# Kernel optimization log

Measured on AMD Instinct MI355X. Metric: run time of the kernel, lower is better.

Reference implementation:

```python
import jax, jax.numpy as jnp
import numpy as np

B = 8          # number of subgraphs (seq_start_end rows)
N = 2048       # nodes per subgraph (equal-size segments)
D = 64         # h_dim
H = 4          # gat_heads
ALPHA = 0.2    # leaky relu slope


def setup_inputs() -> dict:
    key = jax.random.key(0)
    k1, k2, k3, k4, k5 = jax.random.split(key, 5)
    h_states = jax.random.normal(k1, (B * N, D), dtype=jnp.float32)
    # xavier-ish scales
    W_heads = jax.random.normal(k2, (H, D, D), dtype=jnp.float32) * (1.414 * np.sqrt(2.0 / (D + D)))
    a_heads = jax.random.normal(k3, (H, 2 * D), dtype=jnp.float32) * (1.414 * np.sqrt(2.0 / (2 * D + 1)))
    W_out = jax.random.normal(k4, (H * D, D), dtype=jnp.float32) * (1.414 * np.sqrt(2.0 / (H * D + D)))
    a_out = jax.random.normal(k5, (2 * D,), dtype=jnp.float32) * (1.414 * np.sqrt(2.0 / (2 * D + 1)))
    starts = jnp.arange(B, dtype=jnp.int32) * N
    seq_start_end = jnp.stack([starts, starts + N], axis=1)  # (B, 2)
    return {"h_states": h_states, "W_heads": W_heads, "a_heads": a_heads,
            "W_out": W_out, "a_out": a_out, "seq_start_end": seq_start_end}


def _gat_layer(x, W, a):
    """Dense GAT layer. Equivalent to the torch.cat O(N^2*2d) construction,
    rewritten as separate a1/a2 projections + broadcast add. Eval mode (no dropout)."""
    h = x @ W                      # (N, dout)
    d = W.shape[1]
    s1 = h @ a[:d]                 # (N,)  score contribution of source node i
    s2 = h @ a[d:]                 # (N,)  score contribution of target node j
    e = jax.nn.leaky_relu(s1[:, None] + s2[None, :], ALPHA)  # (N, N)
    attn = jax.nn.softmax(e, axis=1)
    return attn @ h                # (N, dout)


def reference(h_states, W_heads, a_heads, W_out, a_out, seq_start_end):
    # seq_start_end encodes B equal contiguous segments of length N -> reshape
    x = h_states.reshape(B, N, D)

    def per_graph(xg):  # xg: (N, D)
        # multi-head attention layers, concat=True -> elu on each head output
        hp = jax.vmap(lambda W, a: jax.nn.elu(_gat_layer(xg, W, a)))(W_heads, a_heads)  # (H, N, D)
        xc = jnp.transpose(hp, (1, 0, 2)).reshape(N, H * D)
        # output attention layer, concat=False (no elu inside), then elu + log_softmax outside
        out = jax.nn.elu(_gat_layer(xc, W_out, a_out))   # (N, D)
        return jax.nn.log_softmax(out, axis=1)

    return jax.vmap(per_graph)(x).reshape(B * N, D)
```

## Files before the change

kernel.cpp:

```cpp
#include <hip/hip_runtime.h>
#include <math.h>

#define NTOT 16384
#define NSEG 2048

#define OFF_HH   0ull
#define OFF_XC   4194304ull
#define OFF_S1H  8388608ull
#define OFF_S2H  8454144ull
#define OFF_S1O  8519680ull
#define OFF_S2O  8536064ull
#define OFF_SVAL 8552448ull
#define OFF_WN   8617984ull
#define OFF_SIDX 8683520ull
#define OFF_VAS  8749056ull
#define OFF_CSA  9277440ull
#define OFF_CSS  9281568ull
#define OFF_SCA  9285696ull
#define OFF_SCS  9351232ull
#define OFF_AS   9416768ull

__device__ inline unsigned long long pack_key(float v, int idx) {
    unsigned u = __float_as_uint(v);
    u = (u & 0x80000000u) ? ~u : (u | 0x80000000u);
    return ((unsigned long long)u << 32) | (unsigned)idx;
}
__device__ inline float unpack_key(unsigned long long k) {
    unsigned u = (unsigned)(k >> 32);
    u = (u & 0x80000000u) ? (u ^ 0x80000000u) : ~u;
    return __uint_as_float(u);
}
__device__ inline unsigned long long shfl_xor_u64(unsigned long long x, int mask) {
    unsigned lo = (unsigned)x, hi = (unsigned)(x >> 32);
    lo = (unsigned)__shfl_xor((int)lo, mask, 64);
    hi = (unsigned)__shfl_xor((int)hi, mask, 64);
    return ((unsigned long long)hi << 32) | lo;
}

__global__ __launch_bounds__(256) void gemm1_k(const float* __restrict__ X,
                                               const float* __restrict__ Wh,
                                               const float* __restrict__ aH,
                                               float* __restrict__ hh,
                                               float* __restrict__ s1h,
                                               float* __restrict__ s2h) {
    __shared__ float As[64][68];
    __shared__ float Bs[64][68];
    const int tid = threadIdx.x;
    const int bm = blockIdx.x, h = blockIdx.y;
    const int c0 = tid & 63, r0 = tid >> 6;
#pragma unroll
    for (int r = 0; r < 16; ++r) {
        int row = r0 + r * 4;
        As[c0][row] = X[(size_t)(bm * 64 + row) * 64 + c0];
        Bs[row][c0] = Wh[h * 4096 + row * 64 + c0];
    }
    __syncthreads();
    const int tx = tid & 15, ty = tid >> 4;
    const int m0 = ty * 4, n0 = tx * 4;
    float acc[4][4] = {};
#pragma unroll
    for (int kk = 0; kk < 64; ++kk) {
        float4 a = *(const float4*)&As[kk][m0];
        float4 b = *(const float4*)&Bs[kk][n0];
        acc[0][0] += a.x * b.x; acc[0][1] += a.x * b.y; acc[0][2] += a.x * b.z; acc[0][3] += a.x * b.w;
        acc[1][0] += a.y * b.x; acc[1][1] += a.y * b.y; acc[1][2] += a.y * b.z; acc[1][3] += a.y * b.w;
        acc[2][0] += a.z * b.x; acc[2][1] += a.z * b.y; acc[2][2] += a.z * b.z; acc[2][3] += a.z * b.w;
        acc[3][0] += a.w * b.x; acc[3][1] += a.w * b.y; acc[3][2] += a.w * b.z; acc[3][3] += a.w * b.w;
    }
    const int g = bm >> 5;
    const int nb = (bm * 64) & 2047;
#pragma unroll
    for (int i = 0; i < 4; ++i) {
        float4 v = make_float4(acc[i][0], acc[i][1], acc[i][2], acc[i][3]);
        *(float4*)&hh[(((size_t)h * 8 + g) * NSEG + nb + m0 + i) * 64 + n0] = v;
    }
#pragma unroll
    for (int i = 0; i < 4; ++i) {
        float p1 = 0.f, p2 = 0.f;
#pragma unroll
        for (int jj = 0; jj < 4; ++jj) {
            p1 += acc[i][jj] * aH[h * 128 + n0 + jj];
            p2 += acc[i][jj] * aH[h * 128 + 64 + n0 + jj];
        }
#pragma unroll
        for (int off = 8; off; off >>= 1) {
            p1 += __shfl_xor(p1, off, 16);
            p2 += __shfl_xor(p2, off, 16);
        }
        if (tx == 0) {
            s1h[h * NTOT + bm * 64 + m0 + i] = p1;
            s2h[h * NTOT + bm * 64 + m0 + i] = p2;
        }
    }
}

__global__ __launch_bounds__(256) void gemm2_k(const float* __restrict__ XC,
                                               const float* __restrict__ Wo,
                                               const float* __restrict__ aO,
                                               float* __restrict__ hc,
                                               float* __restrict__ s1o,
                                               float* __restrict__ s2o) {
    __shared__ float As[64][34];
    __shared__ float Bs[64][68];
    const int tid = threadIdx.x;
    const int bm = blockIdx.x;
    const int c0 = tid & 63, r0 = tid >> 6;
    const int tx = tid & 15, ty = tid >> 4;
    const int m0 = ty * 2, n0 = tx * 4;
    float acc[2][4] = {};
    for (int kt = 0; kt < 4; ++kt) {
#pragma unroll
        for (int r = 0; r < 8; ++r) {
            int row = r0 + r * 4;
            As[c0][row] = XC[(size_t)(bm * 32 + row) * 256 + kt * 64 + c0];
        }
#pragma unroll
        for (int r = 0; r < 16; ++r) {
            int row = r0 + r * 4;
            Bs[row][c0] = Wo[(kt * 64 + row) * 64 + c0];
        }
        __syncthreads();
#pragma unroll
        for (int kk = 0; kk < 64; ++kk) {
            float2 a = *(const float2*)&As[kk][m0];
            float4 b = *(const float4*)&Bs[kk][n0];
            acc[0][0] += a.x * b.x; acc[0][1] += a.x * b.y; acc[0][2] += a.x * b.z; acc[0][3] += a.x * b.w;
            acc[1][0] += a.y * b.x; acc[1][1] += a.y * b.y; acc[1][2] += a.y * b.z; acc[1][3] += a.y * b.w;
        }
        __syncthreads();
    }
#pragma unroll
    for (int i = 0; i < 2; ++i) {
        float4 v = make_float4(acc[i][0], acc[i][1], acc[i][2], acc[i][3]);
        *(float4*)&hc[(size_t)(bm * 32 + m0 + i) * 64 + n0] = v;
    }
#pragma unroll
    for (int i = 0; i < 2; ++i) {
        float p1 = 0.f, p2 = 0.f;
#pragma unroll
        for (int jj = 0; jj < 4; ++jj) {
            p1 += acc[i][jj] * aO[n0 + jj];
            p2 += acc[i][jj] * aO[64 + n0 + jj];
        }
#pragma unroll
        for (int off = 8; off; off >>= 1) {
            p1 += __shfl_xor(p1, off, 16);
            p2 += __shfl_xor(p2, off, 16);
        }
        if (tx == 0) {
            s1o[bm * 32 + m0 + i] = p1;
            s2o[bm * 32 + m0 + i] = p2;
        }
    }
}

__global__ __launch_bounds__(1024) void sort_k(const float* __restrict__ s2_all,
                                               int heads,
                                               float* __restrict__ g_sval,
                                               int* __restrict__ g_sidx,
                                               float* __restrict__ g_wN) {
    __shared__ unsigned long long sA[2][1024];
    __shared__ unsigned long long sB[2][1024];
    __shared__ float sM2;
    const int tid = threadIdx.x, t = blockIdx.x;
    const int g = t / heads, h = t % heads;
    const float* s2p = s2_all + (size_t)h * NTOT + (size_t)g * NSEG;

    unsigned long long a0 = pack_key(s2p[tid], tid);
    unsigned long long a1 = pack_key(s2p[tid + 1024], tid + 1024);
    int p = 0;
    for (int k = 2; k <= 2048; k <<= 1) {
        const bool up0 = (tid & k) == 0;
        const bool up1 = (((tid + 1024) & k) == 0);
        for (int j = k >> 1; j > 0; j >>= 1) {
            if (j >= 1024) {
                unsigned long long lo = a0 < a1 ? a0 : a1;
                unsigned long long hi = a0 < a1 ? a1 : a0;
                a0 = up0 ? lo : hi;
                a1 = up0 ? hi : lo;
            } else if (j >= 64) {
                sA[p][tid] = a0; sB[p][tid] = a1;
                __syncthreads();
                unsigned long long q0 = sA[p][tid ^ j], q1 = sB[p][tid ^ j];
                bool lower = (tid & j) == 0;
                a0 = ((a0 < q0) == (lower == up0)) ? a0 : q0;
                a1 = ((a1 < q1) == (lower == up1)) ? a1 : q1;
                p ^= 1;
            } else {
                unsigned long long q0 = shfl_xor_u64(a0, j);
                unsigned long long q1 = shfl_xor_u64(a1, j);
                bool lower = (tid & j) == 0;
                a0 = ((a0 < q0) == (lower == up0)) ? a0 : q0;
                a1 = ((a1 < q1) == (lower == up1)) ? a1 : q1;
            }
        }
    }
    float v0 = unpack_key(a0), v1 = unpack_key(a1);
    if (tid == 1023) sM2 = v1;
    __syncthreads();
    const float M2 = sM2;
    int i0 = (int)(unsigned)(a0 & 0xffffffffu);
    int i1 = (int)(unsigned)(a1 & 0xffffffffu);
    float w0 = __expf(0.2f * (v0 - M2));
    float w1 = __expf(0.2f * (v1 - M2));
    size_t o = (size_t)t * NSEG;
    g_sval[o + tid] = v0; g_sval[o + tid + 1024] = v1;
    g_sidx[o + tid] = i0; g_sidx[o + tid + 1024] = i1;
    g_wN[o + tid] = w0;   g_wN[o + tid + 1024] = w1;
}

__global__ __launch_bounds__(256) void tabw_k(const float* __restrict__ V,
                                              int heads, int ntask,
                                              const int* __restrict__ g_sidx,
                                              const float* __restrict__ g_wN,
                                              float* __restrict__ AS,
                                              float* __restrict__ SCA, float* __restrict__ SCS,
                                              float* __restrict__ TAS,
                                              float* __restrict__ TSA, float* __restrict__ TSS) {
    const int L = blockIdx.x + (int)(gridDim.x * blockIdx.y);
    const int xcd = L & 7, slot = L >> 3;
    const int tpx = ntask >> 3;
    const int t = xcd * tpx + (slot >> 5);
    const int u = slot & 31;
    const int wv = threadIdx.x >> 6, lane = threadIdx.x & 63;
    const int c = u * 4 + wv, base = c * 16;
    const int g = t / heads, h = t % heads;
    const int seg = h * (ntask / heads) + g;
    const float* Vp = V + (size_t)seg * NSEG * 64;
    const int* sidx = g_sidx + (size_t)t * NSEG + base;
    const float* wnp = g_wN + (size_t)t * NSEG + base;
    float wn[16], vv[16];
#pragma unroll
    for (int j = 0; j < 16; ++j) wn[j] = wnp[j];
#pragma unroll
    for (int j = 0; j < 16; ++j) vv[j] = Vp[(size_t)sidx[j] * 64 + lane];
    float* ASp = AS + (size_t)t * NSEG * 128;
    float accA = 0.f, scaA = 0.f;
#pragma unroll
    for (int j = 0; j < 16; ++j) {
        size_t pos = base + j;
        ASp[pos * 128 + lane] = accA;
        if (lane == 0) SCA[(size_t)t * NSEG + pos] = scaA;
        accA += wn[j] * vv[j]; scaA += wn[j];
    }
    TAS[((size_t)t * 128 + c) * 128 + lane] = accA;
    if (lane == 0) TSA[t * 128 + c] = scaA;
    float accS = 0.f, scaS = 0.f;
#pragma unroll
    for (int j = 15; j >= 0; --j) {
        float w = wn[j], w2 = w * w, wp = w2 * w2 * w;
        accS += wp * vv[j]; scaS += wp;
        size_t pos = base + j;
        ASp[pos * 128 + 64 + lane] = accS;
        if (lane == 0) SCS[(size_t)t * NSEG + pos] = scaS;
    }
    TAS[((size_t)t * 128 + c) * 128 + 64 + lane] = accS;
    if (lane == 0) TSS[t * 128 + c] = scaS;
}

__global__ __launch_bounds__(256) void scan_k(const float* __restrict__ TAS,
                                              const float* __restrict__ TSA,
                                              const float* __restrict__ TSS,
                                              float* __restrict__ VAS,
                                              float* __restrict__ CSA, float* __restrict__ CSS) {
    const int t = blockIdx.x, tid = threadIdx.x;
    const float* T = TAS + (size_t)t * 128 * 128;
    float* Vo = VAS + (size_t)t * 129 * 128;
    if (tid < 64) {
        float run = 0.f;
#pragma unroll 4
        for (int c = 0; c < 128; ++c) { Vo[c * 128 + tid] = run; run += T[c * 128 + tid]; }
        Vo[128 * 128 + tid] = run;
    } else if (tid < 128) {
        float run = 0.f;
#pragma unroll 4
        for (int c = 127; c >= 0; --c) { Vo[c * 128 + tid] = run; run += T[c * 128 + tid]; }
    } else if (tid == 128) {
        float run = 0.f;
        for (int c = 0; c < 128; ++c) { CSA[t * 129 + c] = run; run += TSA[t * 128 + c]; }
        CSA[t * 129 + 128] = run;
    } else if (tid == 129) {
        float run = 0.f;
        for (int c = 127; c >= 0; --c) { CSS[t * 129 + c] = run; run += TSS[t * 128 + c]; }
    }
}

template <int MODE>
__global__ __launch_bounds__(256) void query_k(const float* __restrict__ s1_all,
                                               float* __restrict__ out,
                                               int heads, int ntask, int ostride,
                                               const float* __restrict__ g_sval,
                                               const float* __restrict__ AS,
                                               const float* __restrict__ SCA, const float* __restrict__ SCS,
                                               const float* __restrict__ VAS,
                                               const float* __restrict__ CSA, const float* __restrict__ CSS) {
    __shared__ float sval[NSEG];
    const int tid = threadIdx.x;
    const int L = blockIdx.x + (int)(gridDim.x * blockIdx.y);
    const int xcd = L & 7, slot = L >> 3;
    const int tpx = ntask >> 3;
    const int t = xcd * tpx + (slot >> 5);
    const int u = slot & 31;
    const int g = t / heads, h = t % heads;
    const float4* sv4 = (const float4*)(g_sval + (size_t)t * NSEG);
    for (int i = tid; i < NSEG / 4; i += 256) ((float4*)sval)[i] = sv4[i];
    __syncthreads();
    const float M2 = sval[NSEG - 1];
    const int lane = tid & 63, wv = tid >> 6;
    const int q0 = u * 64 + wv * 16;
    const float* s1p = s1_all + (size_t)h * NTOT + (size_t)g * NSEG;
    float* outp = out + (size_t)g * NSEG * ostride + h * 64;
    const float* ASp = AS + (size_t)t * NSEG * 128;
    const float* VASp = VAS + (size_t)t * 129 * 128;
    const float* scA = SCA + (size_t)t * NSEG;
    const float* scS = SCS + (size_t)t * NSEG;
    const float* csA = CSA + (size_t)t * 129;
    const float* csS = CSS + (size_t)t * 129;
    int myq = q0 + (lane & 15);
    float s1v = s1p[myq];
    float th = -s1v;
    int lo = 0, hi = NSEG;
    while (lo < hi) { int mid = (lo + hi) >> 1; if (sval[mid] <= th) lo = mid + 1; else hi = mid; }
#pragma unroll 4
    for (int j = 0; j < 16; ++j) {
        int k = __shfl(lo, j, 64);
        float s1q = __shfl(s1v, j, 64);
        float accA, scaA, accS, scaS;
        if (k < NSEG) {
            const int c = k >> 4;
            const float* rowP = ASp + (size_t)k * 128;
            const float* rowC = VASp + (size_t)c * 128;
            accA = rowP[lane] + rowC[lane];
            accS = rowP[64 + lane] + rowC[64 + lane];
            scaA = scA[k] + csA[c];
            scaS = scS[k] + csS[c];
        } else {
            accA = VASp[128 * 128 + lane]; scaA = csA[128];
            accS = 0.f; scaS = 0.f;
        }
        float cc = __expf(-0.8f * fmaxf(s1q + M2, 0.f));
        float o = (accS + cc * accA) / (scaS + cc * scaA);
        o = o > 0.f ? o : expm1f(o);
        int q = q0 + j;
        if (MODE == 0) {
            outp[(size_t)q * ostride + lane] = o;
        } else {
            float m = o;
#pragma unroll
            for (int off = 32; off; off >>= 1) m = fmaxf(m, __shfl_xor(m, off, 64));
            float e = __expf(o - m);
#pragma unroll
            for (int off = 32; off; off >>= 1) e += __shfl_xor(e, off, 64);
            outp[(size_t)q * ostride + lane] = o - m - __logf(e);
        }
    }
}

extern "C" void kernel_launch(void* const* d_in, const int* in_sizes, int n_in,
                              void* d_out, int out_size, void* d_ws, size_t ws_size,
                              hipStream_t stream) {
    const float* h_states = (const float*)d_in[0];
    const float* W_heads = (const float*)d_in[1];
    const float* a_heads = (const float*)d_in[2];
    const float* W_out = (const float*)d_in[3];
    const float* a_out = (const float*)d_in[4];
    float* w = (float*)d_ws;
    float* hh = w + OFF_HH;
    float* xc = w + OFF_XC;
    float* hc = w + OFF_HH;
    float* s1h = w + OFF_S1H;
    float* s2h = w + OFF_S2H;
    float* s1o = w + OFF_S1O;
    float* s2o = w + OFF_S2O;
    float* g_sval = w + OFF_SVAL;
    float* g_wN = w + OFF_WN;
    int* g_sidx = (int*)(w + OFF_SIDX);
    float* TAS = w + OFF_XC;
    float* TSA = w + OFF_XC + 524288;
    float* TSS = w + OFF_XC + 528384;
    float* VAS = w + OFF_VAS;
    float* CSA = w + OFF_CSA;
    float* CSS = w + OFF_CSS;
    float* SCA = w + OFF_SCA;
    float* SCS = w + OFF_SCS;
    float* AS = w + OFF_AS;
    float* outp = (float*)d_out;

    gemm1_k<<<dim3(256, 4), 256, 0, stream>>>(h_states, W_heads, a_heads, hh, s1h, s2h);
    sort_k<<<32, 1024, 0, stream>>>(s2h, 4, g_sval, g_sidx, g_wN);
    tabw_k<<<dim3(32, 32), 256, 0, stream>>>(hh, 4, 32, g_sidx, g_wN, AS, SCA, SCS, TAS, TSA, TSS);
    scan_k<<<32, 256, 0, stream>>>(TAS, TSA, TSS, VAS, CSA, CSS);
    query_k<0><<<dim3(32, 32), 256, 0, stream>>>(s1h, xc, 4, 32, 256, g_sval, AS, SCA, SCS, VAS, CSA, CSS);
    gemm2_k<<<512, 256, 0, stream>>>(xc, W_out, a_out, hc, s1o, s2o);
    sort_k<<<8, 1024, 0, stream>>>(s2o, 1, g_sval, g_sidx, g_wN);
    tabw_k<<<dim3(32, 8), 256, 0, stream>>>(hc, 1, 8, g_sidx, g_wN, AS, SCA, SCS, TAS, TSA, TSS);
    scan_k<<<8, 256, 0, stream>>>(TAS, TSA, TSS, VAS, CSA, CSS);
    query_k<1><<<dim3(32, 8), 256, 0, stream>>>(s1o, outp, 1, 8, 64, g_sval, AS, SCA, SCS, VAS, CSA, CSS);
}
```

Baseline: 199.4 us.

## Drop per-element prefix table, recompute intra-chunk sums in query from gathered rows

The tabw kernel no longer writes a full per-position prefix table (AS/SCA/SCS, 2048x128 per task). It now writes only chunk totals over chunks of 4 sorted positions, which scan turns into 512-entry prefix sums. The query kernel rebuilds the partial chunk by gathering up to 4 value rows and weights at lookup time. This removes a large write and read of intermediate data. In exchange, each query does extra gathers and the serial scan is four times longer (512 chunks instead of 128).

```diff
diff --git a/kernel.cpp b/kernel.cpp
--- a/kernel.cpp
+++ b/kernel.cpp
@@ -3,6 +3,7 @@
 
 #define NTOT 16384
 #define NSEG 2048
+#define NCH 512
 
 #define OFF_HH   0ull
 #define OFF_XC   4194304ull
@@ -13,12 +14,12 @@
 #define OFF_SVAL 8552448ull
 #define OFF_WN   8617984ull
 #define OFF_SIDX 8683520ull
-#define OFF_VAS  8749056ull
-#define OFF_CSA  9277440ull
-#define OFF_CSS  9281568ull
-#define OFF_SCA  9285696ull
-#define OFF_SCS  9351232ull
-#define OFF_AS   9416768ull
+#define OFF_TAS  8749056ull
+#define OFF_TSA  10846208ull
+#define OFF_TSS  10862592ull
+#define OFF_VAS  10878976ull
+#define OFF_CSA  12980224ull
+#define OFF_CSS  12996640ull
 
 __device__ inline unsigned long long pack_key(float v, int idx) {
     unsigned u = __float_as_uint(v);
@@ -213,75 +214,66 @@
                                               int heads, int ntask,
                                               const int* __restrict__ g_sidx,
                                               const float* __restrict__ g_wN,
-                                              float* __restrict__ AS,
-                                              float* __restrict__ SCA, float* __restrict__ SCS,
                                               float* __restrict__ TAS,
-                                              float* __restrict__ TSA, float* __restrict__ TSS) {
+                                              float* __restrict__ TSAa, float* __restrict__ TSSa) {
     const int L = blockIdx.x + (int)(gridDim.x * blockIdx.y);
     const int xcd = L & 7, slot = L >> 3;
     const int tpx = ntask >> 3;
     const int t = xcd * tpx + (slot >> 5);
     const int u = slot & 31;
     const int wv = threadIdx.x >> 6, lane = threadIdx.x & 63;
-    const int c = u * 4 + wv, base = c * 16;
     const int g = t / heads, h = t % heads;
     const int seg = h * (ntask / heads) + g;
     const float* Vp = V + (size_t)seg * NSEG * 64;
-    const int* sidx = g_sidx + (size_t)t * NSEG + base;
-    const float* wnp = g_wN + (size_t)t * NSEG + base;
-    float wn[16], vv[16];
-#pragma unroll
-    for (int j = 0; j < 16; ++j) wn[j] = wnp[j];
-#pragma unroll
-    for (int j = 0; j < 16; ++j) vv[j] = Vp[(size_t)sidx[j] * 64 + lane];
-    float* ASp = AS + (size_t)t * NSEG * 128;
-    float accA = 0.f, scaA = 0.f;
-#pragma unroll
-    for (int j = 0; j < 16; ++j) {
-        size_t pos = base + j;
-        ASp[pos * 128 + lane] = accA;
-        if (lane == 0) SCA[(size_t)t * NSEG + pos] = scaA;
-        accA += wn[j] * vv[j]; scaA += wn[j];
-    }
-    TAS[((size_t)t * 128 + c) * 128 + lane] = accA;
-    if (lane == 0) TSA[t * 128 + c] = scaA;
-    float accS = 0.f, scaS = 0.f;
-#pragma unroll
-    for (int j = 15; j >= 0; --j) {
-        float w = wn[j], w2 = w * w, wp = w2 * w2 * w;
-        accS += wp * vv[j]; scaS += wp;
-        size_t pos = base + j;
-        ASp[pos * 128 + 64 + lane] = accS;
-        if (lane == 0) SCS[(size_t)t * NSEG + pos] = scaS;
-    }
-    TAS[((size_t)t * 128 + c) * 128 + 64 + lane] = accS;
-    if (lane == 0) TSS[t * 128 + c] = scaS;
+#pragma unroll
+    for (int cc = 0; cc < 4; ++cc) {
+        const int c = u * 16 + wv * 4 + cc;
+        const int base = c << 2;
+        const int4 si = *(const int4*)&g_sidx[(size_t)t * NSEG + base];
+        const float4 w4 = *(const float4*)&g_wN[(size_t)t * NSEG + base];
+        float v0 = Vp[(size_t)si.x * 64 + lane];
+        float v1 = Vp[(size_t)si.y * 64 + lane];
+        float v2 = Vp[(size_t)si.z * 64 + lane];
+        float v3 = Vp[(size_t)si.w * 64 + lane];
+        float w0 = w4.x, w1 = w4.y, w2 = w4.z, w3 = w4.w;
+        float p0 = w0 * w0 * w0 * w0 * w0, p1 = w1 * w1 * w1 * w1 * w1;
+        float p2 = w2 * w2 * w2 * w2 * w2, p3 = w3 * w3 * w3 * w3 * w3;
+        float ta = w0 * v0 + w1 * v1 + w2 * v2 + w3 * v3;
+        float ts = p0 * v0 + p1 * v1 + p2 * v2 + p3 * v3;
+        float* row = TAS + ((size_t)t * NCH + c) * 128;
+        row[lane] = ta;
+        row[64 + lane] = ts;
+        if (lane == 0) {
+            TSAa[(size_t)t * NCH + c] = w0 + w1 + w2 + w3;
+            TSSa[(size_t)t * NCH + c] = p0 + p1 + p2 + p3;
+        }
+    }
 }
 
 __global__ __launch_bounds__(256) void scan_k(const float* __restrict__ TAS,
-                                              const float* __restrict__ TSA,
-                                              const float* __restrict__ TSS,
+                                              const float* __restrict__ TSAa,
+                                              const float* __restrict__ TSSa,
                                               float* __restrict__ VAS,
-                                              float* __restrict__ CSA, float* __restrict__ CSS) {
+                                              float* __restrict__ CSAa, float* __restrict__ CSSa) {
     const int t = blockIdx.x, tid = threadIdx.x;
-    const float* T = TAS + (size_t)t * 128 * 128;
-    float* Vo = VAS + (size_t)t * 129 * 128;
+    const float* T = TAS + (size_t)t * NCH * 128;
+    float* Vo = VAS + (size_t)t * (NCH + 1) * 128;
     if (tid < 64) {
         float run = 0.f;
-#pragma unroll 4
-        for (int c = 0; c < 128; ++c) { Vo[c * 128 + tid] = run; run += T[c * 128 + tid]; }
-        Vo[128 * 128 + tid] = run;
+#pragma unroll 8
+        for (int c = 0; c < NCH; ++c) { Vo[(size_t)c * 128 + tid] = run; run += T[(size_t)c * 128 + tid]; }
+        Vo[(size_t)NCH * 128 + tid] = run;
     } else if (tid < 128) {
         float run = 0.f;
-#pragma unroll 4
-        for (int c = 127; c >= 0; --c) { Vo[c * 128 + tid] = run; run += T[c * 128 + tid]; }
+#pragma unroll 8
+        for (int c = NCH - 1; c >= 0; --c) { Vo[(size_t)c * 128 + tid] = run; run += T[(size_t)c * 128 + tid]; }
     } else if (tid == 128) {
         float run = 0.f;
-        for (int c = 0; c < 128; ++c) { CSA[t * 129 + c] = run; run += TSA[t * 128 + c]; }
-        CSA[t * 129 + 128] = run;
+        for (int c = 0; c < NCH; ++c) { CSAa[t * (NCH + 1) + c] = run; run += TSAa[(size_t)t * NCH + c]; }
+        CSAa[t * (NCH + 1) + NCH] = run;
     } else if (tid == 129) {
         float run = 0.f;
-        for (int c = 127; c >= 0; --c) { CSS[t * 129 + c] = run; run += TSS[t * 128 + c]; }
+        for (int c = NCH - 1; c >= 0; --c) { CSSa[t * (NCH + 1) + c] = run; run += TSSa[(size_t)t * NCH + c]; }
     }
 }
 
@@ -290,10 +282,12 @@
                                                float* __restrict__ out,
                                                int heads, int ntask, int ostride,
                                                const float* __restrict__ g_sval,
-                                               const float* __restrict__ AS,
-                                               const float* __restrict__ SCA, const float* __restrict__ SCS,
+                                               const int* __restrict__ g_sidx,
+                                               const float* __restrict__ g_wN,
+                                               const float* __restrict__ V,
                                                const float* __restrict__ VAS,
-                                               const float* __restrict__ CSA, const float* __restrict__ CSS) {
+                                               const float* __restrict__ CSAa,
+                                               const float* __restrict__ CSSa) {
     __shared__ float sval[NSEG];
     const int tid = threadIdx.x;
     const int L = blockIdx.x + (int)(gridDim.x * blockIdx.y);
@@ -302,6 +296,8 @@
     const int t = xcd * tpx + (slot >> 5);
     const int u = slot & 31;
     const int g = t / heads, h = t % heads;
+    const int seg = h * (ntask / heads) + g;
+    const float* Vp = V + (size_t)seg * NSEG * 64;
     const float4* sv4 = (const float4*)(g_sval + (size_t)t * NSEG);
     for (int i = tid; i < NSEG / 4; i += 256) ((float4*)sval)[i] = sv4[i];
     __syncthreads();
@@ -310,12 +306,9 @@
     const int q0 = u * 64 + wv * 16;
     const float* s1p = s1_all + (size_t)h * NTOT + (size_t)g * NSEG;
     float* outp = out + (size_t)g * NSEG * ostride + h * 64;
-    const float* ASp = AS + (size_t)t * NSEG * 128;
-    const float* VASp = VAS + (size_t)t * 129 * 128;
-    const float* scA = SCA + (size_t)t * NSEG;
-    const float* scS = SCS + (size_t)t * NSEG;
-    const float* csA = CSA + (size_t)t * 129;
-    const float* csS = CSS + (size_t)t * 129;
+    const float* VASp = VAS + (size_t)t * (NCH + 1) * 128;
+    const float* csA = CSAa + (size_t)t * (NCH + 1);
+    const float* csS = CSSa + (size_t)t * (NCH + 1);
     int myq = q0 + (lane & 15);
     float s1v = s1p[myq];
     float th = -s1v;
@@ -327,15 +320,24 @@
         float s1q = __shfl(s1v, j, 64);
         float accA, scaA, accS, scaS;
         if (k < NSEG) {
-            const int c = k >> 4;
-            const float* rowP = ASp + (size_t)k * 128;
-            const float* rowC = VASp + (size_t)c * 128;
-            accA = rowP[lane] + rowC[lane];
-            accS = rowP[64 + lane] + rowC[64 + lane];
-            scaA = scA[k] + csA[c];
-            scaS = scS[k] + csS[c];
+            const int c = k >> 2;
+            const int base = c << 2;
+            const float* row = VASp + (size_t)c * 128;
+            accA = row[lane]; accS = row[64 + lane];
+            scaA = csA[c];    scaS = csS[c];
+            const int4 si = *(const int4*)&g_sidx[(size_t)t * NSEG + base];
+            const float4 w4 = *(const float4*)&g_wN[(size_t)t * NSEG + base];
+#pragma unroll
+            for (int jj = 0; jj < 4; ++jj) {
+                int idx = (jj == 0) ? si.x : (jj == 1) ? si.y : (jj == 2) ? si.z : si.w;
+                float wn = (jj == 0) ? w4.x : (jj == 1) ? w4.y : (jj == 2) ? w4.z : w4.w;
+                float v = Vp[(size_t)idx * 64 + lane];
+                float wp = wn * wn * wn * wn * wn;
+                if (base + jj < k) { accA += wn * v; scaA += wn; }
+                else               { accS += wp * v; scaS += wp; }
+            }
         } else {
-            accA = VASp[128 * 128 + lane]; scaA = csA[128];
+            accA = VASp[(size_t)NCH * 128 + lane]; scaA = csA[NCH];
             accS = 0.f; scaS = 0.f;
         }
         float cc = __expf(-0.8f * fmaxf(s1q + M2, 0.f));
@@ -375,25 +377,24 @@
     float* g_sval = w + OFF_SVAL;
     float* g_wN = w + OFF_WN;
     int* g_sidx = (int*)(w + OFF_SIDX);
-    float* TAS = w + OFF_XC;
-    float* TSA = w + OFF_XC + 524288;
-    float* TSS = w + OFF_XC + 528384;
+    float* TAS = w + OFF_TAS;
+    float* TSAa = w + OFF_TSA;
+    float* TSSa = w + OFF_TSS;
     float* VAS = w + OFF_VAS;
-    float* CSA = w + OFF_CSA;
-    float* CSS = w + OFF_CSS;
-    float* SCA = w + OFF_SCA;
-    float* SCS = w + OFF_SCS;
-    float* AS = w + OFF_AS;
+    float* CSAa = w + OFF_CSA;
+    float* CSSa = w + OFF_CSS;
     float* outp = (float*)d_out;
 
     gemm1_k<<<dim3(256, 4), 256, 0, stream>>>(h_states, W_heads, a_heads, hh, s1h, s2h);
     sort_k<<<32, 1024, 0, stream>>>(s2h, 4, g_sval, g_sidx, g_wN);
-    tabw_k<<<dim3(32, 32), 256, 0, stream>>>(hh, 4, 32, g_sidx, g_wN, AS, SCA, SCS, TAS, TSA, TSS);
-    scan_k<<<32, 256, 0, stream>>>(TAS, TSA, TSS, VAS, CSA, CSS);
-    query_k<0><<<dim3(32, 32), 256, 0, stream>>>(s1h, xc, 4, 32, 256, g_sval, AS, SCA, SCS, VAS, CSA, CSS);
+    tabw_k<<<dim3(32, 32), 256, 0, stream>>>(hh, 4, 32, g_sidx, g_wN, TAS, TSAa, TSSa);
+    scan_k<<<32, 256, 0, stream>>>(TAS, TSAa, TSSa, VAS, CSAa, CSSa);
+    query_k<0><<<dim3(32, 32), 256, 0, stream>>>(s1h, xc, 4, 32, 256, g_sval, g_sidx, g_wN,
+                                                 hh, VAS, CSAa, CSSa);
     gemm2_k<<<512, 256, 0, stream>>>(xc, W_out, a_out, hc, s1o, s2o);
     sort_k<<<8, 1024, 0, stream>>>(s2o, 1, g_sval, g_sidx, g_wN);
-    tabw_k<<<dim3(32, 8), 256, 0, stream>>>(hc, 1, 8, g_sidx, g_wN, AS, SCA, SCS, TAS, TSA, TSS);
-    scan_k<<<8, 256, 0, stream>>>(TAS, TSA, TSS, VAS, CSA, CSS);
-    query_k<1><<<dim3(32, 8), 256, 0, stream>>>(s1o, outp, 1, 8, 64, g_sval, AS, SCA, SCS, VAS, CSA, CSS);
-}
+    tabw_k<<<dim3(32, 8), 256, 0, stream>>>(hc, 1, 8, g_sidx, g_wN, TAS, TSAa, TSSa);
+    scan_k<<<8, 256, 0, stream>>>(TAS, TSAa, TSSa, VAS, CSAa, CSSa);
+    query_k<1><<<dim3(32, 8), 256, 0, stream>>>(s1o, outp, 1, 8, 64, g_sval, g_sidx, g_wN,
+                                                hc, VAS, CSAa, CSSa);
+}
```

New measurement: 238.1 us. 1.19x slower.

## Fuse chunk prefix scan into query kernel using shared-memory tables

Applied to the files above, without the earlier changes.

Removes the separate scan_k launches. Each query block now loads the per-task chunk-total table into LDS, scans it in place, and reads the chunk prefixes from shared memory instead of from global VAS/CSA/CSS. Query blocks grow to 1024 threads covering 256 queries each, and the grid shrinks to 256 and 64 blocks. This trades two launches and the global round trip for redundant per-block scans, about 73KB of LDS per block, and fewer resident blocks, especially in the second layer.

```diff
diff --git a/kernel.cpp b/kernel.cpp
--- a/kernel.cpp
+++ b/kernel.cpp
@@ -13,12 +13,12 @@
 #define OFF_SVAL 8552448ull
 #define OFF_WN   8617984ull
 #define OFF_SIDX 8683520ull
-#define OFF_VAS  8749056ull
-#define OFF_CSA  9277440ull
-#define OFF_CSS  9281568ull
 #define OFF_SCA  9285696ull
 #define OFF_SCS  9351232ull
 #define OFF_AS   9416768ull
+#define OFF_TAS  17805376ull
+#define OFF_TSA  18329664ull
+#define OFF_TSS  18333760ull
 
 __device__ inline unsigned long long pack_key(float v, int idx) {
     unsigned u = __float_as_uint(v);
@@ -258,64 +258,60 @@
     if (lane == 0) TSS[t * 128 + c] = scaS;
 }
 
-__global__ __launch_bounds__(256) void scan_k(const float* __restrict__ TAS,
-                                              const float* __restrict__ TSA,
-                                              const float* __restrict__ TSS,
-                                              float* __restrict__ VAS,
-                                              float* __restrict__ CSA, float* __restrict__ CSS) {
-    const int t = blockIdx.x, tid = threadIdx.x;
-    const float* T = TAS + (size_t)t * 128 * 128;
-    float* Vo = VAS + (size_t)t * 129 * 128;
+template <int MODE>
+__global__ __launch_bounds__(1024) void query_k(const float* __restrict__ s1_all,
+                                                float* __restrict__ out,
+                                                int heads, int ntask, int ostride,
+                                                const float* __restrict__ g_sval,
+                                                const float* __restrict__ AS,
+                                                const float* __restrict__ SCA, const float* __restrict__ SCS,
+                                                const float* __restrict__ TAS,
+                                                const float* __restrict__ TSA, const float* __restrict__ TSS) {
+    __shared__ float sval[NSEG];
+    __shared__ float Ts[128 * 128];
+    __shared__ float totA[64];
+    __shared__ float csa[132];
+    __shared__ float css[132];
+    const int tid = threadIdx.x;
+    const int L = blockIdx.x;
+    const int xcd = L & 7, slot = L >> 3;
+    const int tpx = ntask >> 3;
+    const int t = xcd * tpx + (slot >> 3);
+    const int u = slot & 7;
+    const int g = t / heads, h = t % heads;
+    const float4* sv4 = (const float4*)(g_sval + (size_t)t * NSEG);
+    if (tid < 512) ((float4*)sval)[tid] = sv4[tid];
+    const float4* Tg4 = (const float4*)(TAS + (size_t)t * 128 * 128);
+    float4* Ts4 = (float4*)Ts;
+#pragma unroll
+    for (int i = 0; i < 4; ++i) Ts4[tid + i * 1024] = Tg4[tid + i * 1024];
+    __syncthreads();
     if (tid < 64) {
         float run = 0.f;
-#pragma unroll 4
-        for (int c = 0; c < 128; ++c) { Vo[c * 128 + tid] = run; run += T[c * 128 + tid]; }
-        Vo[128 * 128 + tid] = run;
+        for (int c = 0; c < 128; ++c) { float v = Ts[c * 128 + tid]; Ts[c * 128 + tid] = run; run += v; }
+        totA[tid] = run;
     } else if (tid < 128) {
         float run = 0.f;
-#pragma unroll 4
-        for (int c = 127; c >= 0; --c) { Vo[c * 128 + tid] = run; run += T[c * 128 + tid]; }
+        for (int c = 127; c >= 0; --c) { float v = Ts[c * 128 + tid]; Ts[c * 128 + tid] = run; run += v; }
     } else if (tid == 128) {
+        const float* TSAp = TSA + (size_t)t * 128;
         float run = 0.f;
-        for (int c = 0; c < 128; ++c) { CSA[t * 129 + c] = run; run += TSA[t * 128 + c]; }
-        CSA[t * 129 + 128] = run;
+        for (int c = 0; c < 128; ++c) { csa[c] = run; run += TSAp[c]; }
+        csa[128] = run;
     } else if (tid == 129) {
+        const float* TSSp = TSS + (size_t)t * 128;
         float run = 0.f;
-        for (int c = 127; c >= 0; --c) { CSS[t * 129 + c] = run; run += TSS[t * 128 + c]; }
-    }
-}
-
-template <int MODE>
-__global__ __launch_bounds__(256) void query_k(const float* __restrict__ s1_all,
-                                               float* __restrict__ out,
-                                               int heads, int ntask, int ostride,
-                                               const float* __restrict__ g_sval,
-                                               const float* __restrict__ AS,
-                                               const float* __restrict__ SCA, const float* __restrict__ SCS,
-                                               const float* __restrict__ VAS,
-                                               const float* __restrict__ CSA, const float* __restrict__ CSS) {
-    __shared__ float sval[NSEG];
-    const int tid = threadIdx.x;
-    const int L = blockIdx.x + (int)(gridDim.x * blockIdx.y);
-    const int xcd = L & 7, slot = L >> 3;
-    const int tpx = ntask >> 3;
-    const int t = xcd * tpx + (slot >> 5);
-    const int u = slot & 31;
-    const int g = t / heads, h = t % heads;
-    const float4* sv4 = (const float4*)(g_sval + (size_t)t * NSEG);
-    for (int i = tid; i < NSEG / 4; i += 256) ((float4*)sval)[i] = sv4[i];
+        for (int c = 127; c >= 0; --c) { css[c] = run; run += TSSp[c]; }
+    }
     __syncthreads();
     const float M2 = sval[NSEG - 1];
     const int lane = tid & 63, wv = tid >> 6;
-    const int q0 = u * 64 + wv * 16;
+    const int q0 = u * 256 + wv * 16;
     const float* s1p = s1_all + (size_t)h * NTOT + (size_t)g * NSEG;
     float* outp = out + (size_t)g * NSEG * ostride + h * 64;
     const float* ASp = AS + (size_t)t * NSEG * 128;
-    const float* VASp = VAS + (size_t)t * 129 * 128;
     const float* scA = SCA + (size_t)t * NSEG;
     const float* scS = SCS + (size_t)t * NSEG;
-    const float* csA = CSA + (size_t)t * 129;
-    const float* csS = CSS + (size_t)t * 129;
     int myq = q0 + (lane & 15);
     float s1v = s1p[myq];
     float th = -s1v;
@@ -329,13 +325,12 @@
         if (k < NSEG) {
             const int c = k >> 4;
             const float* rowP = ASp + (size_t)k * 128;
-            const float* rowC = VASp + (size_t)c * 128;
-            accA = rowP[lane] + rowC[lane];
-            accS = rowP[64 + lane] + rowC[64 + lane];
-            scaA = scA[k] + csA[c];
-            scaS = scS[k] + csS[c];
+            accA = rowP[lane]      + Ts[c * 128 + lane];
+            accS = rowP[64 + lane] + Ts[c * 128 + 64 + lane];
+            scaA = scA[k] + csa[c];
+            scaS = scS[k] + css[c];
         } else {
-            accA = VASp[128 * 128 + lane]; scaA = csA[128];
+            accA = totA[lane]; scaA = csa[128];
             accS = 0.f; scaS = 0.f;
         }
         float cc = __expf(-0.8f * fmaxf(s1q + M2, 0.f));
@@ -375,25 +370,20 @@
     float* g_sval = w + OFF_SVAL;
     float* g_wN = w + OFF_WN;
     int* g_sidx = (int*)(w + OFF_SIDX);
-    float* TAS = w + OFF_XC;
-    float* TSA = w + OFF_XC + 524288;
-    float* TSS = w + OFF_XC + 528384;
-    float* VAS = w + OFF_VAS;
-    float* CSA = w + OFF_CSA;
-    float* CSS = w + OFF_CSS;
     float* SCA = w + OFF_SCA;
     float* SCS = w + OFF_SCS;
     float* AS = w + OFF_AS;
+    float* TAS = w + OFF_TAS;
+    float* TSA = w + OFF_TSA;
+    float* TSS = w + OFF_TSS;
     float* outp = (float*)d_out;
 
     gemm1_k<<<dim3(256, 4), 256, 0, stream>>>(h_states, W_heads, a_heads, hh, s1h, s2h);
     sort_k<<<32, 1024, 0, stream>>>(s2h, 4, g_sval, g_sidx, g_wN);
     tabw_k<<<dim3(32, 32), 256, 0, stream>>>(hh, 4, 32, g_sidx, g_wN, AS, SCA, SCS, TAS, TSA, TSS);
-    scan_k<<<32, 256, 0, stream>>>(TAS, TSA, TSS, VAS, CSA, CSS);
-    query_k<0><<<dim3(32, 32), 256, 0, stream>>>(s1h, xc, 4, 32, 256, g_sval, AS, SCA, SCS, VAS, CSA, CSS);
+    query_k<0><<<256, 1024, 0, stream>>>(s1h, xc, 4, 32, 256, g_sval, AS, SCA, SCS, TAS, TSA, TSS);
     gemm2_k<<<512, 256, 0, stream>>>(xc, W_out, a_out, hc, s1o, s2o);
     sort_k<<<8, 1024, 0, stream>>>(s2o, 1, g_sval, g_sidx, g_wN);
     tabw_k<<<dim3(32, 8), 256, 0, stream>>>(hc, 1, 8, g_sidx, g_wN, AS, SCA, SCS, TAS, TSA, TSS);
-    scan_k<<<8, 256, 0, stream>>>(TAS, TSA, TSS, VAS, CSA, CSS);
-    query_k<1><<<dim3(32, 8), 256, 0, stream>>>(s1o, outp, 1, 8, 64, g_sval, AS, SCA, SCS, VAS, CSA, CSS);
-}
+    query_k<1><<<64, 1024, 0, stream>>>(s1o, outp, 1, 8, 64, g_sval, AS, SCA, SCS, TAS, TSA, TSS);
+}
```

Measured after the change: 182.4 us. -8.5%, faster.
